# Performance work log

Measured on AMD Instinct MI355X. Metric: run time of the kernel, lower is better.

## Reference

```python
import jax, jax.numpy as jnp
import numpy as np

D_MODEL, N_HEAD, N_KV_HEAD, D_HEAD = 1024, 16, 4, 64


def rotate_half(x):
    x1, x2 = x[..., : x.shape[-1] // 2], x[..., x.shape[-1] // 2:]
    return jnp.concatenate((-x2, x1), axis=-1)


def rope_cos_sin(seq_len, dim, dtype=jnp.float32):
    inv_freq = 1.0 / (10000.0 ** (jnp.arange(0, dim, 2, dtype=jnp.float32) / dim))
    t = jnp.arange(seq_len, dtype=jnp.float32)
    freqs = jnp.einsum('i,j->ij', t, inv_freq)          # [S, dim/2]
    emb = jnp.concatenate((freqs, freqs), axis=-1)       # [S, dim]
    return jnp.cos(emb).astype(dtype), jnp.sin(emb).astype(dtype)


def setup_inputs() -> dict:
    key = jax.random.key(0)
    ks = jax.random.split(key, 5)
    B, S = 2, 2048
    scale = 0.02
    return {
        'x': jax.random.normal(ks[0], (B, S, D_MODEL), dtype=jnp.float32),
        'Wq': jax.random.normal(ks[1], (D_MODEL, N_HEAD * D_HEAD), dtype=jnp.float32) * scale,
        'Wk': jax.random.normal(ks[2], (D_MODEL, N_KV_HEAD * D_HEAD), dtype=jnp.float32) * scale,
        'Wv': jax.random.normal(ks[3], (D_MODEL, N_KV_HEAD * D_HEAD), dtype=jnp.float32) * scale,
        'Wo': jax.random.normal(ks[4], (N_HEAD * D_HEAD, D_MODEL), dtype=jnp.float32) * scale,
    }


def reference(x, Wq, Wk, Wv, Wo):
    B, S, _ = x.shape
    scale = 1.0 / np.sqrt(D_HEAD)
    # projections -> [B, H, S, Dh]
    q = (x @ Wq).reshape(B, S, N_HEAD, D_HEAD).transpose(0, 2, 1, 3)
    k = (x @ Wk).reshape(B, S, N_KV_HEAD, D_HEAD).transpose(0, 2, 1, 3)
    v = (x @ Wv).reshape(B, S, N_KV_HEAD, D_HEAD).transpose(0, 2, 1, 3)
    cos, sin = rope_cos_sin(S, D_HEAD, x.dtype)          # [S, Dh]
    q = q * cos + rotate_half(q) * sin
    k = k * cos + rotate_half(k) * sin
    rep = N_HEAD // N_KV_HEAD
    k = jnp.repeat(k, rep, axis=1)                       # [B, H, S, Dh]
    v = jnp.repeat(v, rep, axis=1)
    scores = jnp.einsum('bhqd,bhkd->bhqk', q, k) * scale # [B, H, S, S]
    causal = jnp.triu(jnp.ones((S, S), dtype=bool), k=1)
    scores = jnp.where(causal, -jnp.inf, scores)
    probs = jax.nn.softmax(scores, axis=-1)
    ctx = jnp.einsum('bhqk,bhkd->bhqd', probs, v)        # [B, H, S, Dh]
    ctx = ctx.transpose(0, 2, 1, 3).reshape(B, S, N_HEAD * D_HEAD)
    return ctx @ Wo
```

## Files before the change

### kernel.cpp

```cpp
#include <hip/hip_runtime.h>
#include <hip/hip_bf16.h>
#include <cstdint>
#include <math.h>

#define S_LEN 2048
#define DM 1024
#define NQKV 1536
#define MROWS 4096
#define BKT 64

typedef __attribute__((ext_vector_type(8))) short short8;
typedef __attribute__((ext_vector_type(4))) float f32x4;
typedef __attribute__((ext_vector_type(16))) float f32x16;

#define QFOLD 0.18033688011112042f

__device__ __forceinline__ short f2bf(float x) {
  union { float f; uint32_t u; } v; v.f = x;
  uint32_t r = (v.u + 0x7fffu + ((v.u >> 16) & 1u)) >> 16;
  return (short)(uint16_t)r;
}

__device__ __forceinline__ uint32_t pk2(float a, float b) {
  __hip_bfloat162 h = __float22bfloat162_rn(make_float2(a, b));
  union { __hip_bfloat162 h2; uint32_t u; } cv; cv.h2 = h;
  return cv.u;
}

__global__ __launch_bounds__(256) void prep(const float* __restrict__ x,
    const float* __restrict__ Wq, const float* __restrict__ Wk,
    const float* __restrict__ Wv, const float* __restrict__ Wo,
    short* __restrict__ Xb, short* __restrict__ WcatT, short* __restrict__ WoT,
    float2* __restrict__ tab) {
  __shared__ short T[64 * 72];
  const int bb = blockIdx.x;
  const int tid = threadIdx.x;
  if (bb < 4096) {
    const int i = bb * 256 + tid;
    float4 v = ((const float4*)x)[i];
    short4 o;
    o.x = f2bf(v.x); o.y = f2bf(v.y); o.z = f2bf(v.z); o.w = f2bf(v.w);
    ((short4*)Xb)[i] = o;
    return;
  }
  if (bb >= 4736) {
    const int gid = (bb - 4736) * 256 + tid;
    #pragma unroll
    for (int e = 0; e < 4; ++e) {
      const int ii = gid + e * 16384;
      const int s = ii >> 5, j = ii & 31;
      const float inv = exp2f(-(float)j * 0.41524101186092029f);
      const float ang = (float)s * inv;
      tab[ii] = make_float2(cosf(ang), sinf(ang));
    }
    return;
  }
  const float* src; short* dst; int R, C, t2 = bb - 4096;
  if (t2 < 256)      { src = Wq; dst = WcatT;                        R = 1024; C = 1024; }
  else if (t2 < 320) { t2 -= 256; src = Wk; dst = WcatT + (size_t)1024*1024; R = 1024; C = 256; }
  else if (t2 < 384) { t2 -= 320; src = Wv; dst = WcatT + (size_t)1280*1024; R = 1024; C = 256; }
  else               { t2 -= 384; src = Wo; dst = WoT;               R = 1024; C = 1024; }
  const int r0 = (t2 & 15) * 64, c0 = (t2 >> 4) * 64;
  #pragma unroll
  for (int i = 0; i < 4; ++i) {
    int chunk = tid + i * 256;
    int r = chunk >> 4, cc = (chunk & 15) * 4;
    float4 v = *(const float4*)&src[(size_t)(r0 + r) * C + c0 + cc];
    T[(cc + 0) * 72 + r] = f2bf(v.x);
    T[(cc + 1) * 72 + r] = f2bf(v.y);
    T[(cc + 2) * 72 + r] = f2bf(v.z);
    T[(cc + 3) * 72 + r] = f2bf(v.w);
  }
  __syncthreads();
  #pragma unroll
  for (int i = 0; i < 2; ++i) {
    int chunk = tid + i * 256;
    int rr = chunk >> 3, kk = (chunk & 7) * 8;
    *(uint4*)&dst[(size_t)(c0 + rr) * R + r0 + kk] = *(uint4*)&T[rr * 72 + kk];
  }
}

template<int BMT, int BNT>
__global__ __launch_bounds__(256) void gemm_bf16_t(const short* __restrict__ A,
    const short* __restrict__ BT, float* __restrict__ C, int M, int N, int K) {
  constexpr int MI = BMT / 32, NI = BNT / 32;
  __shared__ short As[BMT * BKT];
  __shared__ short Bs[BNT * BKT];
  const int tid = threadIdx.x;
  const int wave = tid >> 6, lane = tid & 63;
  const int quad = lane >> 4, l15 = lane & 15;
  const int wm = (wave >> 1) * (BMT / 2), wn = (wave & 1) * (BNT / 2);
  const int m0 = blockIdx.y * BMT, n0 = blockIdx.x * BNT;
  const int rA = wave * (BMT / 4) + (lane >> 3);
  const int rB = wave * (BNT / 4) + (lane >> 3);
  const int scol = (lane & 7) * 8;

  f32x4 acc[MI][NI] = {};

  for (int k0 = 0; k0 < K; k0 += BKT) {
    __syncthreads();
    #pragma unroll
    for (int j = 0; j < MI; ++j)
      __builtin_amdgcn_global_load_lds(
          (const __attribute__((address_space(1))) void*)&A[(size_t)(m0 + rA + j * 8) * K + k0 + scol],
          (__attribute__((address_space(3))) void*)&As[(wave * MI + j) * 512],
          16, 0, 0);
    #pragma unroll
    for (int j = 0; j < NI; ++j)
      __builtin_amdgcn_global_load_lds(
          (const __attribute__((address_space(1))) void*)&BT[(size_t)(n0 + rB + j * 8) * K + k0 + scol],
          (__attribute__((address_space(3))) void*)&Bs[(wave * NI + j) * 512],
          16, 0, 0);
    __syncthreads();
    #pragma unroll
    for (int ks = 0; ks < 2; ++ks) {
      short8 af[MI], bfr[NI];
      #pragma unroll
      for (int mi = 0; mi < MI; ++mi)
        af[mi] = *(const short8*)&As[(wm + mi*16 + l15)*BKT + ks*32 + quad*8];
      #pragma unroll
      for (int ni = 0; ni < NI; ++ni)
        bfr[ni] = *(const short8*)&Bs[(wn + ni*16 + l15)*BKT + ks*32 + quad*8];
      #pragma unroll
      for (int mi = 0; mi < MI; ++mi)
        #pragma unroll
        for (int ni = 0; ni < NI; ++ni)
          acc[mi][ni] = __builtin_amdgcn_mfma_f32_16x16x32_bf16(af[mi], bfr[ni], acc[mi][ni], 0, 0, 0);
    }
  }
  #pragma unroll
  for (int mi = 0; mi < MI; ++mi)
    #pragma unroll
    for (int ni = 0; ni < NI; ++ni)
      #pragma unroll
      for (int r = 0; r < 4; ++r)
        C[(size_t)(m0 + wm + mi*16 + quad*4 + r)*N + (n0 + wn + ni*16 + l15)] = acc[mi][ni][r];
}

__global__ __launch_bounds__(256, 3) void gemm_qkv(const short* __restrict__ A,
    const short* __restrict__ BT, const float2* __restrict__ tab,
    short* __restrict__ Qb, short* __restrict__ Kb, short* __restrict__ Vb) {
  constexpr int MI = 2, NI = 4;
  __shared__ short As[64 * BKT];
  __shared__ short Bs[128 * BKT];
  const int tid = threadIdx.x;
  const int wave = tid >> 6, lane = tid & 63;
  const int quad = lane >> 4, l15 = lane & 15;
  const int wm = (wave >> 1) * 32, wn = (wave & 1) * 64;
  const int m0 = blockIdx.y * 64, n0 = blockIdx.x * 128;
  const int rA = wave * 16 + (lane >> 3);
  const int rB = wave * 32 + (lane >> 3);
  const int scol = (lane & 7) * 8;

  f32x4 acc[MI][NI] = {};

  for (int k0 = 0; k0 < DM; k0 += BKT) {
    __syncthreads();
    #pragma unroll
    for (int j = 0; j < MI; ++j)
      __builtin_amdgcn_global_load_lds(
          (const __attribute__((address_space(1))) void*)&A[(size_t)(m0 + rA + j * 8) * DM + k0 + scol],
          (__attribute__((address_space(3))) void*)&As[(wave * MI + j) * 512],
          16, 0, 0);
    #pragma unroll
    for (int j = 0; j < NI; ++j)
      __builtin_amdgcn_global_load_lds(
          (const __attribute__((address_space(1))) void*)&BT[(size_t)(n0 + rB + j * 8) * DM + k0 + scol],
          (__attribute__((address_space(3))) void*)&Bs[(wave * NI + j) * 512],
          16, 0, 0);
    __syncthreads();
    #pragma unroll
    for (int ks = 0; ks < 2; ++ks) {
      short8 af[MI], bfr[NI];
      #pragma unroll
      for (int mi = 0; mi < MI; ++mi)
        af[mi] = *(const short8*)&As[(wm + mi*16 + l15)*BKT + ks*32 + quad*8];
      #pragma unroll
      for (int ni = 0; ni < NI; ++ni)
        bfr[ni] = *(const short8*)&Bs[(wn + ni*16 + l15)*BKT + ks*32 + quad*8];
      #pragma unroll
      for (int mi = 0; mi < MI; ++mi)
        #pragma unroll
        for (int ni = 0; ni < NI; ++ni)
          acc[mi][ni] = __builtin_amdgcn_mfma_f32_16x16x32_bf16(af[mi], bfr[ni], acc[mi][ni], 0, 0, 0);
    }
  }

  const int c0 = n0 + wn;
  if (n0 < 1024) {
    #pragma unroll
    for (int mi = 0; mi < MI; ++mi)
      #pragma unroll
      for (int r = 0; r < 4; ++r) {
        const int row = m0 + wm + mi*16 + quad*4 + r;
        const int s = row & (S_LEN - 1);
        #pragma unroll
        for (int ni = 0; ni < 2; ++ni) {
          const int j = ni*16 + l15;
          const float2 cn = tab[s*32 + j];
          const float x1 = acc[mi][ni][r], x2 = acc[mi][ni+2][r];
          Qb[(size_t)row*1024 + c0 + j]      = f2bf((x1*cn.x - x2*cn.y) * QFOLD);
          Qb[(size_t)row*1024 + c0 + j + 32] = f2bf((x2*cn.x + x1*cn.y) * QFOLD);
        }
      }
  } else if (n0 < 1280) {
    const int hh = (c0 - 1024) >> 6;
    #pragma unroll
    for (int mi = 0; mi < MI; ++mi)
      #pragma unroll
      for (int r = 0; r < 4; ++r) {
        const int row = m0 + wm + mi*16 + quad*4 + r;
        const int s = row & (S_LEN - 1);
        const int sw = (s & 7) << 3;
        #pragma unroll
        for (int ni = 0; ni < 2; ++ni) {
          const int j = ni*16 + l15;
          const float2 cn = tab[s*32 + j];
          const float x1 = acc[mi][ni][r], x2 = acc[mi][ni+2][r];
          Kb[(size_t)row*256 + hh*64 + (j ^ sw)]        = f2bf(x1*cn.x - x2*cn.y);
          Kb[(size_t)row*256 + hh*64 + ((j + 32) ^ sw)] = f2bf(x2*cn.x + x1*cn.y);
        }
      }
  } else {
    #pragma unroll
    for (int mi = 0; mi < MI; ++mi)
      #pragma unroll
      for (int ni = 0; ni < NI; ++ni)
        #pragma unroll
        for (int r = 0; r < 4; ++r) {
          const int row = m0 + wm + mi*16 + quad*4 + r;
          Vb[(size_t)row*256 + (c0 - 1280) + ni*16 + l15] = f2bf(acc[mi][ni][r]);
        }
  }
}

__global__ __launch_bounds__(256) void transpose_v(const short* __restrict__ Vb,
                                                   short* __restrict__ Vt) {
  __shared__ short T[64 * 72];
  const int s0 = blockIdx.x * 64;
  const int bh = blockIdx.y;
  const int b = bh >> 2, kvh = bh & 3;
  const int tid = threadIdx.x;
  #pragma unroll
  for (int i = 0; i < 2; ++i) {
    int chunk = tid + i * 256;
    int r = chunk >> 3, c = (chunk & 7) * 8;
    short8 v = *(const short8*)&Vb[(size_t)(b*S_LEN + s0 + r)*256 + kvh*64 + c];
    #pragma unroll
    for (int t = 0; t < 8; ++t) T[(c + t) * 72 + r] = v[t];
  }
  __syncthreads();
  #pragma unroll
  for (int i = 0; i < 2; ++i) {
    int chunk = tid + i * 256;
    int rr = chunk >> 3, kk = (chunk & 7) * 8;
    *(uint4*)&Vt[(size_t)(bh*64 + rr)*S_LEN + s0 + (kk ^ ((rr & 7) << 3))] = *(uint4*)&T[rr * 72 + kk];
  }
}

__global__ __launch_bounds__(256, 3) void fattn11(const short* __restrict__ Qb,
    const short* __restrict__ Kb, const short* __restrict__ Vt, short* __restrict__ Ctx) {
  __shared__ short SMEM[24576];
  const int idx = blockIdx.x;
  const int h   = idx & 15;
  const int b   = (idx >> 4) & 1;
  const int jt  = 31 - (idx >> 5);
  const int kvh = h >> 2;
  const int tid = threadIdx.x, wav = tid >> 6, lane = tid & 63;
  const int l31 = lane & 31, hi = lane >> 5;
  const int qs = wav & 1, g = wav >> 1;
  const int sx = (l31 & 7) << 3;
  const size_t qbase  = (size_t)b * S_LEN * 1024;
  const size_t kbase  = (size_t)b * S_LEN * 256;
  const size_t vtbase = (size_t)(b * 4 + kvh) * 64 * S_LEN;

  const short* kptr = Kb + kbase + (size_t)(wav * 16 + (lane >> 3)) * 256 + kvh * 64 + (lane & 7) * 8;
  const short* vptr = Vt + vtbase + (size_t)(wav * 16 + (lane >> 3)) * 2048 + (lane & 7) * 8;

#define STAGE(u) do { \
    const int bi_ = (u) % 3; \
    const short* kp_ = kptr + (size_t)(u) * 16384; \
    const short* vp_ = vptr + (u) * 64; \
    short* kd_ = &SMEM[bi_ * 8192 + wav * 1024]; \
    short* vd_ = &SMEM[bi_ * 8192 + 4096 + wav * 1024]; \
    _Pragma("unroll") \
    for (int i_ = 0; i_ < 2; ++i_) { \
      __builtin_amdgcn_global_load_lds((const __attribute__((address_space(1))) void*)(kp_ + i_ * 2048), \
          (__attribute__((address_space(3))) void*)(kd_ + i_ * 512), 16, 0, 0); \
      __builtin_amdgcn_global_load_lds((const __attribute__((address_space(1))) void*)(vp_ + i_ * 16384), \
          (__attribute__((address_space(3))) void*)(vd_ + i_ * 512), 16, 0, 0); \
    } \
  } while (0)

  const int q0 = jt * 64;
  const int ntiles = jt + 1;
  const int qg = q0 + qs * 32 + l31;

  short8 qf[4];
  {
    const short* qp = &Qb[qbase + (size_t)qg * 1024 + h * 64 + hi * 8];
    #pragma unroll
    for (int ks = 0; ks < 4; ++ks) qf[ks] = *(const short8*)(qp + ks * 16);
  }

  f32x16 O0 = {}, O1 = {};
  float la0 = 0.f, la1 = 0.f, la2 = 0.f, la3 = 0.f;

  STAGE(0);
  if (ntiles > 1) STAGE(1);

  for (int t = 0; t < ntiles; ++t) {
    const int k0 = t * 64;
    const int rem = ntiles - 1 - t;
    if (rem >= 1) { asm volatile("s_waitcnt vmcnt(4)" ::: "memory"); }
    else          { asm volatile("s_waitcnt vmcnt(0)" ::: "memory"); }
    __builtin_amdgcn_sched_barrier(0);
    __builtin_amdgcn_s_barrier();
    if (t + 2 < ntiles) STAGE(t + 2);

    const short* ks_ = &SMEM[(t % 3) * 8192];
    const short* vs_ = &SMEM[(t % 3) * 8192 + 4096];

    f32x16 sc;
    __builtin_amdgcn_s_setprio(1);
    {
      const int r = g * 32 + l31;
      f32x16 a = {};
      #pragma unroll
      for (int ks2 = 0; ks2 < 4; ++ks2) {
        short8 kf = *(const short8*)&ks_[r * 64 + ((ks2 * 16 + hi * 8) ^ sx)];
        a = __builtin_amdgcn_mfma_f32_32x32x16_bf16(kf, qf[ks2], a, 0, 0, 0);
      }
      sc = a;
    }
    __builtin_amdgcn_s_setprio(0);

    if (t == ntiles - 1) {
      #pragma unroll
      for (int r = 0; r < 16; ++r) {
        const int kvg = k0 + g * 32 + (r & 3) + 8 * (r >> 2) + 4 * hi;
        if (kvg > qg) sc[r] = -1e30f;
      }
    }

    short8 af[2];
    {
      #pragma unroll
      for (int r = 0; r < 16; ++r) sc[r] = exp2f(sc[r]);
      la0 += (sc[0] + sc[1]) + (sc[2] + sc[3]);
      la1 += (sc[4] + sc[5]) + (sc[6] + sc[7]);
      la2 += (sc[8] + sc[9]) + (sc[10] + sc[11]);
      la3 += (sc[12] + sc[13]) + (sc[14] + sc[15]);
      #pragma unroll
      for (int st = 0; st < 2; ++st) {
        uint32_t x0 = pk2(sc[st * 8 + 0], sc[st * 8 + 1]);
        uint32_t x1 = pk2(sc[st * 8 + 2], sc[st * 8 + 3]);
        uint32_t x2 = pk2(sc[st * 8 + 4], sc[st * 8 + 5]);
        uint32_t x3 = pk2(sc[st * 8 + 6], sc[st * 8 + 7]);
        asm("v_permlane32_swap_b32 %0, %1" : "+v"(x0), "+v"(x2));
        asm("v_permlane32_swap_b32 %0, %1" : "+v"(x1), "+v"(x3));
        union { short8 s8; uint32_t u[4]; } cv;
        cv.u[0] = x0; cv.u[1] = x1; cv.u[2] = x2; cv.u[3] = x3;
        af[st] = cv.s8;
      }
    }

    __builtin_amdgcn_s_setprio(1);
    #pragma unroll
    for (int s2 = 0; s2 < 2; ++s2) {
      const int co = g * 32 + s2 * 16 + hi * 8;
      short8 bv0 = *(const short8*)&vs_[l31 * 64 + (co ^ sx)];
      O0 = __builtin_amdgcn_mfma_f32_32x32x16_bf16(af[s2], bv0, O0, 0, 0, 0);
      short8 bv1 = *(const short8*)&vs_[(32 + l31) * 64 + (co ^ sx)];
      O1 = __builtin_amdgcn_mfma_f32_32x32x16_bf16(af[s2], bv1, O1, 0, 0, 0);
    }
    __builtin_amdgcn_s_setprio(0);
  }

  float ll = (la0 + la1) + (la2 + la3);
  ll += __shfl_xor(ll, 32, 64);
  __syncthreads();

  float* Os = (float*)SMEM;
  float* Ls = (float*)SMEM + 2 * 64 * 33;
  if (g == 1) {
    float* op = &Os[(qs * 64 + lane) * 33];
    #pragma unroll
    for (int r = 0; r < 16; ++r) { op[r] = O0[r]; op[16 + r] = O1[r]; }
    Ls[qs * 64 + lane] = ll;
  }
  __syncthreads();
  if (g == 0) {
    const float* op = &Os[(qs * 64 + lane) * 33];
    ll += Ls[qs * 64 + lane];
    #pragma unroll
    for (int r = 0; r < 16; ++r) { O0[r] += op[r]; O1[r] += op[16 + r]; }
    const float inv = 1.0f / ll;
    #pragma unroll
    for (int r = 0; r < 16; ++r) {
      const int crow = (r & 3) + 8 * (r >> 2) + 4 * hi;
      const float invr = __shfl(inv, crow, 64);
      const size_t o = qbase + (size_t)(q0 + qs * 32 + crow) * 1024 + h * 64;
      Ctx[o + l31]      = f2bf(O0[r] * invr);
      Ctx[o + 32 + l31] = f2bf(O1[r] * invr);
    }
  }
#undef STAGE
}

extern "C" void kernel_launch(void* const* d_in, const int* in_sizes, int n_in,
                              void* d_out, int out_size, void* d_ws, size_t ws_size,
                              hipStream_t stream) {
  const float* x  = (const float*)d_in[0];
  const float* Wq = (const float*)d_in[1];
  const float* Wk = (const float*)d_in[2];
  const float* Wv = (const float*)d_in[3];
  const float* Wo = (const float*)d_in[4];
  float* out = (float*)d_out;

  char* w = (char*)d_ws;
  short*  Xb    = (short*)w;   w += (size_t)MROWS * DM * 2;
  short*  WcatT = (short*)w;   w += (size_t)NQKV * DM * 2;
  short*  WoT   = (short*)w;   w += (size_t)DM * DM * 2;
  short*  Qbuf  = (short*)w;   w += (size_t)MROWS * DM * 2;
  short*  Kbuf  = (short*)w;   w += (size_t)MROWS * 256 * 2;
  short*  Vbuf  = (short*)w;   w += (size_t)MROWS * 256 * 2;
  short*  Vt    = (short*)w;   w += (size_t)8 * 64 * S_LEN * 2;
  short*  Ctx   = (short*)w;   w += (size_t)MROWS * DM * 2;
  float2* tab   = (float2*)w;  w += (size_t)S_LEN * 32 * 8;

  prep<<<dim3(4800), dim3(256), 0, stream>>>(x, Wq, Wk, Wv, Wo, Xb, WcatT, WoT, tab);

  gemm_qkv<<<dim3(NQKV / 128, MROWS / 64), dim3(256), 0, stream>>>(Xb, WcatT, tab, Qbuf, Kbuf, Vbuf);
  transpose_v<<<dim3(32, 8), dim3(256), 0, stream>>>(Vbuf, Vt);
  fattn11<<<dim3(1024), dim3(256), 0, stream>>>(Qbuf, Kbuf, Vt, Ctx);
  gemm_bf16_t<64,128><<<dim3(DM / 128, MROWS / 64), dim3(256), 0, stream>>>(Ctx, WoT, out, MROWS, DM, DM);
}
```

Measured before the change: 164.5 us.

## Fuse V transpose into QKV GEMM epilogue and split attention MFMA chains

The QKV GEMM epilogue for V columns now stages the tile through shared memory and writes V directly in transposed, swizzled layout. This removes the separate transpose_v kernel, its launch, and the intermediate Vbuf round trip. The attention kernel also splits the QK^T and PV MFMA accumulation into two independent chains that are summed at the end, shortening dependent MFMA latency. The cost is extra accumulator registers, which may pressure occupancy, plus extra syncs in the GEMM epilogue.

```diff
diff --git a/kernel.cpp b/kernel.cpp
--- a/kernel.cpp
+++ b/kernel.cpp
@@ -139,10 +139,11 @@
 
 __global__ __launch_bounds__(256, 3) void gemm_qkv(const short* __restrict__ A,
     const short* __restrict__ BT, const float2* __restrict__ tab,
-    short* __restrict__ Qb, short* __restrict__ Kb, short* __restrict__ Vb) {
+    short* __restrict__ Qb, short* __restrict__ Kb, short* __restrict__ Vt) {
   constexpr int MI = 2, NI = 4;
-  __shared__ short As[64 * BKT];
-  __shared__ short Bs[128 * BKT];
+  __shared__ short SM[12288];
+  short* As = SM;
+  short* Bs = SM + 4096;
   const int tid = threadIdx.x;
   const int wave = tid >> 6, lane = tid & 63;
   const int quad = lane >> 4, l15 = lane & 15;
@@ -222,43 +223,32 @@
         }
       }
   } else {
+    __syncthreads();
     #pragma unroll
     for (int mi = 0; mi < MI; ++mi)
       #pragma unroll
-      for (int ni = 0; ni < NI; ++ni)
-        #pragma unroll
-        for (int r = 0; r < 4; ++r) {
-          const int row = m0 + wm + mi*16 + quad*4 + r;
-          Vb[(size_t)row*256 + (c0 - 1280) + ni*16 + l15] = f2bf(acc[mi][ni][r]);
-        }
-  }
-}
-
-__global__ __launch_bounds__(256) void transpose_v(const short* __restrict__ Vb,
-                                                   short* __restrict__ Vt) {
-  __shared__ short T[64 * 72];
-  const int s0 = blockIdx.x * 64;
-  const int bh = blockIdx.y;
-  const int b = bh >> 2, kvh = bh & 3;
-  const int tid = threadIdx.x;
-  #pragma unroll
-  for (int i = 0; i < 2; ++i) {
-    int chunk = tid + i * 256;
-    int r = chunk >> 3, c = (chunk & 7) * 8;
-    short8 v = *(const short8*)&Vb[(size_t)(b*S_LEN + s0 + r)*256 + kvh*64 + c];
-    #pragma unroll
-    for (int t = 0; t < 8; ++t) T[(c + t) * 72 + r] = v[t];
-  }
-  __syncthreads();
-  #pragma unroll
-  for (int i = 0; i < 2; ++i) {
-    int chunk = tid + i * 256;
-    int rr = chunk >> 3, kk = (chunk & 7) * 8;
-    *(uint4*)&Vt[(size_t)(bh*64 + rr)*S_LEN + s0 + (kk ^ ((rr & 7) << 3))] = *(uint4*)&T[rr * 72 + kk];
-  }
-}
-
-__global__ __launch_bounds__(256, 3) void fattn11(const short* __restrict__ Qb,
+      for (int ni = 0; ni < NI; ++ni) {
+        short4 p;
+        p.x = f2bf(acc[mi][ni][0]); p.y = f2bf(acc[mi][ni][1]);
+        p.z = f2bf(acc[mi][ni][2]); p.w = f2bf(acc[mi][ni][3]);
+        *(short4*)&SM[(wn + ni*16 + l15)*80 + wm + mi*16 + quad*4] = p;
+      }
+    __syncthreads();
+    const int b_ = m0 >> 11, sbase = m0 & (S_LEN - 1);
+    #pragma unroll
+    for (int i = 0; i < 4; ++i) {
+      const int chunk = tid + i * 256;
+      const int vl = chunk >> 3;
+      const int kk = (chunk & 7) * 8;
+      const int vcol = (n0 - 1280) + vl;
+      const int kvh = vcol >> 6, dd = vcol & 63;
+      uint4 v = *(uint4*)&SM[vl*80 + kk];
+      *(uint4*)&Vt[((size_t)((b_*4 + kvh)*64 + dd))*S_LEN + sbase + (kk ^ ((dd & 7) << 3))] = v;
+    }
+  }
+}
+
+__global__ __launch_bounds__(256, 3) void fattn12(const short* __restrict__ Qb,
     const short* __restrict__ Kb, const short* __restrict__ Vt, short* __restrict__ Ctx) {
   __shared__ short SMEM[24576];
   const int idx = blockIdx.x;
@@ -304,6 +294,7 @@
   }
 
   f32x16 O0 = {}, O1 = {};
+  f32x16 P0 = {}, P1 = {};
   float la0 = 0.f, la1 = 0.f, la2 = 0.f, la3 = 0.f;
 
   STAGE(0);
@@ -325,13 +316,17 @@
     __builtin_amdgcn_s_setprio(1);
     {
       const int r = g * 32 + l31;
-      f32x16 a = {};
-      #pragma unroll
-      for (int ks2 = 0; ks2 < 4; ++ks2) {
-        short8 kf = *(const short8*)&ks_[r * 64 + ((ks2 * 16 + hi * 8) ^ sx)];
-        a = __builtin_amdgcn_mfma_f32_32x32x16_bf16(kf, qf[ks2], a, 0, 0, 0);
-      }
-      sc = a;
+      short8 kf0 = *(const short8*)&ks_[r * 64 + ((0 * 16 + hi * 8) ^ sx)];
+      short8 kf1 = *(const short8*)&ks_[r * 64 + ((1 * 16 + hi * 8) ^ sx)];
+      short8 kf2 = *(const short8*)&ks_[r * 64 + ((2 * 16 + hi * 8) ^ sx)];
+      short8 kf3 = *(const short8*)&ks_[r * 64 + ((3 * 16 + hi * 8) ^ sx)];
+      f32x16 a0 = {}, a1 = {};
+      a0 = __builtin_amdgcn_mfma_f32_32x32x16_bf16(kf0, qf[0], a0, 0, 0, 0);
+      a1 = __builtin_amdgcn_mfma_f32_32x32x16_bf16(kf2, qf[2], a1, 0, 0, 0);
+      a0 = __builtin_amdgcn_mfma_f32_32x32x16_bf16(kf1, qf[1], a0, 0, 0, 0);
+      a1 = __builtin_amdgcn_mfma_f32_32x32x16_bf16(kf3, qf[3], a1, 0, 0, 0);
+      #pragma unroll
+      for (int r2 = 0; r2 < 16; ++r2) sc[r2] = a0[r2] + a1[r2];
     }
     __builtin_amdgcn_s_setprio(0);
 
@@ -366,16 +361,23 @@
     }
 
     __builtin_amdgcn_s_setprio(1);
-    #pragma unroll
-    for (int s2 = 0; s2 < 2; ++s2) {
-      const int co = g * 32 + s2 * 16 + hi * 8;
-      short8 bv0 = *(const short8*)&vs_[l31 * 64 + (co ^ sx)];
-      O0 = __builtin_amdgcn_mfma_f32_32x32x16_bf16(af[s2], bv0, O0, 0, 0, 0);
-      short8 bv1 = *(const short8*)&vs_[(32 + l31) * 64 + (co ^ sx)];
-      O1 = __builtin_amdgcn_mfma_f32_32x32x16_bf16(af[s2], bv1, O1, 0, 0, 0);
+    {
+      const int co0 = g * 32 + hi * 8;
+      const int co1 = g * 32 + 16 + hi * 8;
+      short8 bv00 = *(const short8*)&vs_[l31 * 64 + (co0 ^ sx)];
+      short8 bv01 = *(const short8*)&vs_[(32 + l31) * 64 + (co0 ^ sx)];
+      short8 bv10 = *(const short8*)&vs_[l31 * 64 + (co1 ^ sx)];
+      short8 bv11 = *(const short8*)&vs_[(32 + l31) * 64 + (co1 ^ sx)];
+      O0 = __builtin_amdgcn_mfma_f32_32x32x16_bf16(af[0], bv00, O0, 0, 0, 0);
+      O1 = __builtin_amdgcn_mfma_f32_32x32x16_bf16(af[0], bv01, O1, 0, 0, 0);
+      P0 = __builtin_amdgcn_mfma_f32_32x32x16_bf16(af[1], bv10, P0, 0, 0, 0);
+      P1 = __builtin_amdgcn_mfma_f32_32x32x16_bf16(af[1], bv11, P1, 0, 0, 0);
     }
     __builtin_amdgcn_s_setprio(0);
   }
+
+  #pragma unroll
+  for (int r = 0; r < 16; ++r) { O0[r] += P0[r]; O1[r] += P1[r]; }
 
   float ll = (la0 + la1) + (la2 + la3);
   ll += __shfl_xor(ll, 32, 64);
@@ -424,15 +426,13 @@
   short*  WoT   = (short*)w;   w += (size_t)DM * DM * 2;
   short*  Qbuf  = (short*)w;   w += (size_t)MROWS * DM * 2;
   short*  Kbuf  = (short*)w;   w += (size_t)MROWS * 256 * 2;
-  short*  Vbuf  = (short*)w;   w += (size_t)MROWS * 256 * 2;
   short*  Vt    = (short*)w;   w += (size_t)8 * 64 * S_LEN * 2;
   short*  Ctx   = (short*)w;   w += (size_t)MROWS * DM * 2;
   float2* tab   = (float2*)w;  w += (size_t)S_LEN * 32 * 8;
 
   prep<<<dim3(4800), dim3(256), 0, stream>>>(x, Wq, Wk, Wv, Wo, Xb, WcatT, WoT, tab);
 
-  gemm_qkv<<<dim3(NQKV / 128, MROWS / 64), dim3(256), 0, stream>>>(Xb, WcatT, tab, Qbuf, Kbuf, Vbuf);
-  transpose_v<<<dim3(32, 8), dim3(256), 0, stream>>>(Vbuf, Vt);
-  fattn11<<<dim3(1024), dim3(256), 0, stream>>>(Qbuf, Kbuf, Vt, Ctx);
+  gemm_qkv<<<dim3(NQKV / 128, MROWS / 64), dim3(256), 0, stream>>>(Xb, WcatT, tab, Qbuf, Kbuf, Vt);
+  fattn12<<<dim3(1024), dim3(256), 0, stream>>>(Qbuf, Kbuf, Vt, Ctx);
   gemm_bf16_t<64,128><<<dim3(DM / 128, MROWS / 64), dim3(256), 0, stream>>>(Ctx, WoT, out, MROWS, DM, DM);
 }
```

Measured after the change: 164.2 us. No clear change (-0.2%).
